# Kernel tuning notes

Measured on AMD Instinct MI355X. Metric: run time of the kernel, lower is better.

Reference implementation:

```python
import jax, jax.numpy as jnp
import numpy as np

B, S, D = 4, 4096, 256


def setup_inputs() -> dict:
    key = jax.random.key(0)
    ks = jax.random.split(key, 8)
    inv = 1.0 / np.sqrt(D)
    return {
        "input_tensor": jax.random.normal(ks[0], (B, S, D), dtype=jnp.float32),
        "attention_mask": jax.random.randint(ks[1], (B, S, S), 0, 2) == 1,
        "Wq": jax.random.uniform(ks[2], (D, D), jnp.float32, -inv, inv),
        "bq": jax.random.uniform(ks[3], (D,), jnp.float32, -inv, inv),
        "Wk": jax.random.uniform(ks[4], (D, D), jnp.float32, -inv, inv),
        "bk": jax.random.uniform(ks[5], (D,), jnp.float32, -inv, inv),
        "Wv": jax.random.uniform(ks[6], (D, D), jnp.float32, -inv, inv),
        "bv": jax.random.uniform(ks[7], (D,), jnp.float32, -inv, inv),
    }


def reference(input_tensor, attention_mask, Wq, bq, Wk, bk, Wv, bv):
    # Linear projections: y = x @ W.T + b  (nn.Linear convention, W is [out,in])
    query = jnp.einsum("bsd,ed->bse", input_tensor, Wq) + bq
    key = jnp.einsum("bsd,ed->bse", input_tensor, Wk) + bk
    value = jnp.einsum("bsd,ed->bse", input_tensor, Wv) + bv
    # Faithful quirk: original scales by sqrt(query.size(1)) == sqrt(seq_len)
    scale = jnp.asarray(query.shape[1], query.dtype) ** 0.5
    scores = jnp.einsum("bqd,bkd->bqk", query, key) / scale  # [B,S,S]
    scores = jnp.where(attention_mask, jnp.asarray(-1e9, scores.dtype), scores)
    attn = jax.nn.softmax(scores, axis=-1)
    # dropout with p=0.0 is identity (eval-mode reference)
    context = jnp.einsum("bqk,bkd->bqd", attn, value)
    return context
```

## Files before the change

kernel.cpp:

```cpp
#include <hip/hip_runtime.h>
#include <hip/hip_bf16.h>
#include <stdint.h>

#define BB 4
#define SS 4096
#define DD 256

typedef __attribute__((ext_vector_type(4))) float f32x4;
typedef __attribute__((ext_vector_type(8))) short s16x8;

__device__ __forceinline__ ushort f2bf(float f) {
  __hip_bfloat16 h = __float2bfloat16(f);
  return __builtin_bit_cast(ushort, h);
}

__global__ void convert_kernel(const float* __restrict__ X,
                               const float* __restrict__ Wq,
                               const float* __restrict__ Wk,
                               const float* __restrict__ Wv,
                               const float* __restrict__ bq,
                               const float* __restrict__ bk,
                               const float* __restrict__ bv,
                               ushort* __restrict__ Xb,
                               ushort* __restrict__ Wb,
                               float* __restrict__ bias) {
  int tid = blockIdx.x * blockDim.x + threadIdx.x;
  int stride = gridDim.x * blockDim.x;
  const int NX4 = (BB * SS * DD) / 4;
  for (int i = tid; i < NX4; i += stride) {
    float4 v = ((const float4*)X)[i];
    ushort4 o = { f2bf(v.x), f2bf(v.y), f2bf(v.z), f2bf(v.w) };
    ((ushort4*)Xb)[i] = o;
  }
  const int NW4 = (DD * DD) / 4;
  for (int i = tid; i < NW4; i += stride) {
    float4 a = ((const float4*)Wq)[i];
    float4 b = ((const float4*)Wk)[i];
    float4 c = ((const float4*)Wv)[i];
    ushort4 oa = { f2bf(a.x), f2bf(a.y), f2bf(a.z), f2bf(a.w) };
    ushort4 ob = { f2bf(b.x), f2bf(b.y), f2bf(b.z), f2bf(b.w) };
    ushort4 oc = { f2bf(c.x), f2bf(c.y), f2bf(c.z), f2bf(c.w) };
    ((ushort4*)Wb)[i]           = oa;
    ((ushort4*)Wb)[NW4 + i]     = ob;
    ((ushort4*)Wb)[2 * NW4 + i] = oc;
  }
  if (tid < DD) {
    bias[tid]          = bq[tid];
    bias[DD + tid]     = bk[tid];
    bias[2 * DD + tid] = bv[tid];
  }
}

#define LROW 40

__global__ __launch_bounds__(256) void proj_gemm(const ushort* __restrict__ Xb,
                                                 const ushort* __restrict__ Wb,
                                                 const float* __restrict__ bias,
                                                 ushort* __restrict__ Qb,
                                                 ushort* __restrict__ Kb,
                                                 ushort* __restrict__ Vt) {
  __shared__ ushort Al[128 * LROW];
  __shared__ ushort Bl[128 * LROW];
  const int m0 = blockIdx.x * 128;
  const int n0 = blockIdx.y * 128;
  const int t = threadIdx.x;
  const int lane = t & 63;
  const int w = t >> 6;
  const int wr = w & 1, wc = w >> 1;
  const int col = lane & 15;
  const int quad = lane >> 4;

  f32x4 acc[4][4];
#pragma unroll
  for (int i = 0; i < 4; i++)
#pragma unroll
    for (int j = 0; j < 4; j++) acc[i][j] = f32x4{0.f, 0.f, 0.f, 0.f};

  const int ci0 = t, ci1 = 256 + t;
  const int r0 = ci0 >> 2, c0 = ci0 & 3;
  const int r1 = ci1 >> 2, c1 = ci1 & 3;

  s16x8 pa0 = *(const s16x8*)(Xb + (m0 + r0) * DD + c0 * 8);
  s16x8 pa1 = *(const s16x8*)(Xb + (m0 + r1) * DD + c1 * 8);
  s16x8 pb0 = *(const s16x8*)(Wb + (n0 + r0) * DD + c0 * 8);
  s16x8 pb1 = *(const s16x8*)(Wb + (n0 + r1) * DD + c1 * 8);

  for (int kk = 0; kk < DD; kk += 32) {
    __syncthreads();
    *(s16x8*)&Al[r0 * LROW + c0 * 8] = pa0;
    *(s16x8*)&Al[r1 * LROW + c1 * 8] = pa1;
    *(s16x8*)&Bl[r0 * LROW + c0 * 8] = pb0;
    *(s16x8*)&Bl[r1 * LROW + c1 * 8] = pb1;
    __syncthreads();
    const int kn = kk + 32;
    if (kn < DD) {
      pa0 = *(const s16x8*)(Xb + (m0 + r0) * DD + kn + c0 * 8);
      pa1 = *(const s16x8*)(Xb + (m0 + r1) * DD + kn + c1 * 8);
      pb0 = *(const s16x8*)(Wb + (n0 + r0) * DD + kn + c0 * 8);
      pb1 = *(const s16x8*)(Wb + (n0 + r1) * DD + kn + c1 * 8);
    }
    s16x8 af[4], bfr[4];
#pragma unroll
    for (int mi = 0; mi < 4; mi++)
      af[mi] = *(const s16x8*)&Al[(wr * 64 + mi * 16 + col) * LROW + quad * 8];
#pragma unroll
    for (int ni = 0; ni < 4; ni++)
      bfr[ni] = *(const s16x8*)&Bl[(wc * 64 + ni * 16 + col) * LROW + quad * 8];
#pragma unroll
    for (int mi = 0; mi < 4; mi++)
#pragma unroll
      for (int ni = 0; ni < 4; ni++)
        acc[mi][ni] = __builtin_amdgcn_mfma_f32_16x16x32_bf16(af[mi], bfr[ni], acc[mi][ni], 0, 0, 0);
  }

  const int region = n0 >> 8;
#pragma unroll
  for (int mi = 0; mi < 4; mi++) {
    const int gm = m0 + wr * 64 + mi * 16 + quad * 4;
#pragma unroll
    for (int ni = 0; ni < 4; ni++) {
      const int gn = n0 + wc * 64 + ni * 16 + col;
      const float bb = bias[gn];
      f32x4 v = acc[mi][ni];
      if (region == 0) {
#pragma unroll
        for (int rg = 0; rg < 4; rg++)
          Qb[(gm + rg) * DD + gn] = f2bf((v[rg] + bb) * 0.015625f);
      } else if (region == 1) {
        const int d = gn - 256;
#pragma unroll
        for (int rg = 0; rg < 4; rg++)
          Kb[(gm + rg) * DD + d] = f2bf(v[rg] + bb);
      } else {
        const int d = gn - 512;
        const int b = gm >> 12;
        const int s = gm & (SS - 1);
        ushort4 o = { f2bf(v[0] + bb), f2bf(v[1] + bb), f2bf(v[2] + bb), f2bf(v[3] + bb) };
        *(ushort4*)&Vt[((size_t)(b << 8) + d) * SS + s] = o;
      }
    }
  }
}

#define NKT 32
#define KROW 264
#define VROW 40
#define PROW 40

__global__ __launch_bounds__(256) void attn_kernel(const ushort* __restrict__ Qb,
                                                   const ushort* __restrict__ Kb,
                                                   const ushort* __restrict__ Vt,
                                                   const int* __restrict__ mask,
                                                   float* __restrict__ out) {
  __shared__ ushort Kl[NKT * KROW];
  __shared__ ushort Vl[DD * VROW];
  __shared__ ushort Pl[4][16 * PROW];

  const int qt = blockIdx.x;
  const int b = blockIdx.y;
  const int t = threadIdx.x;
  const int lane = t & 63;
  const int w = t >> 6;
  const int col = lane & 15;
  const int quad = lane >> 4;

  const int q0 = qt * 64;
  const int qrow = q0 + w * 16;

  s16x8 qf[8];
  {
    const ushort* qp = Qb + ((size_t)b * SS + qrow + col) * DD + quad * 8;
#pragma unroll
    for (int dc = 0; dc < 8; dc++) qf[dc] = *(const s16x8*)(qp + dc * 32);
  }

  int kr[4], kc[4], vd[4], vc[4];
#pragma unroll
  for (int i = 0; i < 4; i++) {
    const int ci = i * 256 + t;
    kr[i] = ci >> 5; kc[i] = ci & 31;
    vd[i] = ci >> 2; vc[i] = ci & 3;
  }

  const ushort* Kg = Kb + (size_t)b * SS * DD;
  const ushort* Vg = Vt + (size_t)b * DD * SS;
  const int* Mg = mask + ((size_t)b * SS + q0 + w * 16 + quad * 4) * SS;

  f32x4 Oc[16];
#pragma unroll
  for (int i = 0; i < 16; i++) Oc[i] = f32x4{0.f, 0.f, 0.f, 0.f};
  float m_i[4] = {-INFINITY, -INFINITY, -INFINITY, -INFINITY};
  float l_i[4] = {0.f, 0.f, 0.f, 0.f};

  s16x8 pk[4], pv[4];
  int pm[2][4];
#pragma unroll
  for (int i = 0; i < 4; i++) {
    pk[i] = *(const s16x8*)(Kg + (size_t)kr[i] * DD + kc[i] * 8);
    pv[i] = *(const s16x8*)(Vg + (size_t)vd[i] * SS + vc[i] * 8);
  }
#pragma unroll
  for (int jt = 0; jt < 2; jt++)
#pragma unroll
    for (int rg = 0; rg < 4; rg++) pm[jt][rg] = Mg[rg * SS + jt * 16 + col];

  const int NT = SS / NKT;
  for (int tt = 0; tt < NT; tt++) {
    __syncthreads();
#pragma unroll
    for (int i = 0; i < 4; i++) {
      *(s16x8*)&Kl[kr[i] * KROW + kc[i] * 8] = pk[i];
      *(s16x8*)&Vl[vd[i] * VROW + vc[i] * 8] = pv[i];
    }
    __syncthreads();
    int mcur[2][4];
#pragma unroll
    for (int jt = 0; jt < 2; jt++)
#pragma unroll
      for (int rg = 0; rg < 4; rg++) mcur[jt][rg] = pm[jt][rg];
    if (tt + 1 < NT) {
      const int k0n = (tt + 1) * NKT;
#pragma unroll
      for (int i = 0; i < 4; i++) {
        pk[i] = *(const s16x8*)(Kg + ((size_t)k0n + kr[i]) * DD + kc[i] * 8);
        pv[i] = *(const s16x8*)(Vg + (size_t)vd[i] * SS + k0n + vc[i] * 8);
      }
#pragma unroll
      for (int jt = 0; jt < 2; jt++)
#pragma unroll
        for (int rg = 0; rg < 4; rg++) pm[jt][rg] = Mg[rg * SS + k0n + jt * 16 + col];
    }

    f32x4 st[2];
#pragma unroll
    for (int jt = 0; jt < 2; jt++) {
      f32x4 s = f32x4{0.f, 0.f, 0.f, 0.f};
#pragma unroll
      for (int dc = 0; dc < 8; dc++) {
        s16x8 kb = *(const s16x8*)&Kl[(jt * 16 + col) * KROW + dc * 32 + quad * 8];
        s = __builtin_amdgcn_mfma_f32_16x16x32_bf16(qf[dc], kb, s, 0, 0, 0);
      }
      st[jt] = s;
    }
#pragma unroll
    for (int jt = 0; jt < 2; jt++)
#pragma unroll
      for (int rg = 0; rg < 4; rg++)
        if (mcur[jt][rg]) st[jt][rg] = -1e9f;

    float al[4];
#pragma unroll
    for (int rg = 0; rg < 4; rg++) {
      float v = fmaxf(st[0][rg], st[1][rg]);
      v = fmaxf(v, __shfl_xor(v, 1));
      v = fmaxf(v, __shfl_xor(v, 2));
      v = fmaxf(v, __shfl_xor(v, 4));
      v = fmaxf(v, __shfl_xor(v, 8));
      const float mn = fmaxf(m_i[rg], v);
      al[rg] = __expf(m_i[rg] - mn);
      m_i[rg] = mn;
    }
#pragma unroll
    for (int rg = 0; rg < 4; rg++) {
      const float p0 = __expf(st[0][rg] - m_i[rg]);
      const float p1 = __expf(st[1][rg] - m_i[rg]);
      st[0][rg] = p0; st[1][rg] = p1;
      float s2 = p0 + p1;
      s2 += __shfl_xor(s2, 1);
      s2 += __shfl_xor(s2, 2);
      s2 += __shfl_xor(s2, 4);
      s2 += __shfl_xor(s2, 8);
      l_i[rg] = l_i[rg] * al[rg] + s2;
    }
#pragma unroll
    for (int dt = 0; dt < 16; dt++)
#pragma unroll
      for (int rg = 0; rg < 4; rg++) Oc[dt][rg] *= al[rg];

#pragma unroll
    for (int jt = 0; jt < 2; jt++)
#pragma unroll
      for (int rg = 0; rg < 4; rg++)
        Pl[w][(quad * 4 + rg) * PROW + jt * 16 + col] = f2bf(st[jt][rg]);
    s16x8 pa = *(const s16x8*)&Pl[w][col * PROW + quad * 8];

#pragma unroll
    for (int dt = 0; dt < 16; dt++) {
      s16x8 vb = *(const s16x8*)&Vl[(dt * 16 + col) * VROW + quad * 8];
      Oc[dt] = __builtin_amdgcn_mfma_f32_16x16x32_bf16(pa, vb, Oc[dt], 0, 0, 0);
    }
  }

  float inv[4];
#pragma unroll
  for (int rg = 0; rg < 4; rg++) inv[rg] = 1.0f / l_i[rg];
  float* op = out + ((size_t)b * SS + qrow + quad * 4) * DD;
#pragma unroll
  for (int dt = 0; dt < 16; dt++)
#pragma unroll
    for (int rg = 0; rg < 4; rg++)
      op[rg * DD + dt * 16 + col] = Oc[dt][rg] * inv[rg];
}

extern "C" void kernel_launch(void* const* d_in, const int* in_sizes, int n_in,
                              void* d_out, int out_size, void* d_ws, size_t ws_size,
                              hipStream_t stream) {
  const float* X  = (const float*)d_in[0];
  const int* mask = (const int*)d_in[1];
  const float* Wq = (const float*)d_in[2];
  const float* bq = (const float*)d_in[3];
  const float* Wk = (const float*)d_in[4];
  const float* bk = (const float*)d_in[5];
  const float* Wv = (const float*)d_in[6];
  const float* bv = (const float*)d_in[7];
  float* out = (float*)d_out;

  ushort* base = (ushort*)d_ws;
  ushort* Xb = base;
  ushort* Wb = Xb + (size_t)BB * SS * DD;
  ushort* Qb = Wb + (size_t)3 * DD * DD;
  ushort* Kb = Qb + (size_t)BB * SS * DD;
  ushort* Vt = Kb + (size_t)BB * SS * DD;
  float* bias = (float*)(Vt + (size_t)BB * SS * DD);

  convert_kernel<<<1024, 256, 0, stream>>>(X, Wq, Wk, Wv, bq, bk, bv, Xb, Wb, bias);
  proj_gemm<<<dim3(128, 6), 256, 0, stream>>>(Xb, Wb, bias, Qb, Kb, Vt);
  attn_kernel<<<dim3(64, 4), 256, 0, stream>>>(Qb, Kb, Vt, mask, out);
}
```

Measured before the change: 619.1 us.

## Split key range across two wave groups per block and merge softmax partials

Doubles the attention block to 512 threads, with each 256-thread group processing half of the key sequence using its own K/V LDS buffers. At the end, group 1 writes its running max, sum and output accumulators to LDS, and group 0 rescales and merges them before writing the output. This is meant to raise waves per CU, since the grid has only one block per CU, to better hide memory and MFMA latency. It also sets wave priority around the MFMA loops. The larger block tightens the per-thread register budget and adds a merge step.

```diff
diff --git a/kernel.cpp b/kernel.cpp
--- a/kernel.cpp
+++ b/kernel.cpp
@@ -147,22 +147,36 @@
 #define VROW 40
 #define PROW 40
 
-__global__ __launch_bounds__(256) void attn_kernel(const ushort* __restrict__ Qb,
+#define KL_U (NKT * KROW)
+#define VL_U (DD * VROW)
+#define PL_U (16 * PROW)
+#define VOFF (2 * KL_U)
+#define POFF (VOFF + 2 * VL_U)
+#define SM_U (POFF + 8 * PL_U)
+
+#define XSTRIDE 72
+
+__global__ __launch_bounds__(512) void attn_kernel(const ushort* __restrict__ Qb,
                                                    const ushort* __restrict__ Kb,
                                                    const ushort* __restrict__ Vt,
                                                    const int* __restrict__ mask,
                                                    float* __restrict__ out) {
-  __shared__ ushort Kl[NKT * KROW];
-  __shared__ ushort Vl[DD * VROW];
-  __shared__ ushort Pl[4][16 * PROW];
+  __shared__ __align__(16) ushort sm[SM_U];
 
   const int qt = blockIdx.x;
   const int b = blockIdx.y;
   const int t = threadIdx.x;
+  const int g = t >> 8;
+  const int tg = t & 255;
   const int lane = t & 63;
-  const int w = t >> 6;
+  const int w = tg >> 6;
+  const int w8 = t >> 6;
   const int col = lane & 15;
   const int quad = lane >> 4;
+
+  ushort* Kl = sm + g * KL_U;
+  ushort* Vl = sm + VOFF + g * VL_U;
+  ushort* Pw = sm + POFF + w8 * PL_U;
 
   const int q0 = qt * 64;
   const int qrow = q0 + w * 16;
@@ -177,14 +191,14 @@
   int kr[4], kc[4], vd[4], vc[4];
 #pragma unroll
   for (int i = 0; i < 4; i++) {
-    const int ci = i * 256 + t;
+    const int ci = i * 256 + tg;
     kr[i] = ci >> 5; kc[i] = ci & 31;
     vd[i] = ci >> 2; vc[i] = ci & 3;
   }
 
   const ushort* Kg = Kb + (size_t)b * SS * DD;
   const ushort* Vg = Vt + (size_t)b * DD * SS;
-  const int* Mg = mask + ((size_t)b * SS + q0 + w * 16 + quad * 4) * SS;
+  const int* Mg = mask + ((size_t)b * SS + qrow + quad * 4) * SS;
 
   f32x4 Oc[16];
 #pragma unroll
@@ -192,20 +206,22 @@
   float m_i[4] = {-INFINITY, -INFINITY, -INFINITY, -INFINITY};
   float l_i[4] = {0.f, 0.f, 0.f, 0.f};
 
+  const int NT2 = (SS / NKT) / 2;
+  const int kb0 = g * NT2 * NKT;
+
   s16x8 pk[4], pv[4];
   int pm[2][4];
 #pragma unroll
   for (int i = 0; i < 4; i++) {
-    pk[i] = *(const s16x8*)(Kg + (size_t)kr[i] * DD + kc[i] * 8);
-    pv[i] = *(const s16x8*)(Vg + (size_t)vd[i] * SS + vc[i] * 8);
+    pk[i] = *(const s16x8*)(Kg + (size_t)(kb0 + kr[i]) * DD + kc[i] * 8);
+    pv[i] = *(const s16x8*)(Vg + (size_t)vd[i] * SS + kb0 + vc[i] * 8);
   }
 #pragma unroll
   for (int jt = 0; jt < 2; jt++)
 #pragma unroll
-    for (int rg = 0; rg < 4; rg++) pm[jt][rg] = Mg[rg * SS + jt * 16 + col];
-
-  const int NT = SS / NKT;
-  for (int tt = 0; tt < NT; tt++) {
+    for (int rg = 0; rg < 4; rg++) pm[jt][rg] = Mg[rg * SS + kb0 + jt * 16 + col];
+
+  for (int tt = 0; tt < NT2; tt++) {
     __syncthreads();
 #pragma unroll
     for (int i = 0; i < 4; i++) {
@@ -218,8 +234,8 @@
     for (int jt = 0; jt < 2; jt++)
 #pragma unroll
       for (int rg = 0; rg < 4; rg++) mcur[jt][rg] = pm[jt][rg];
-    if (tt + 1 < NT) {
-      const int k0n = (tt + 1) * NKT;
+    if (tt + 1 < NT2) {
+      const int k0n = kb0 + (tt + 1) * NKT;
 #pragma unroll
       for (int i = 0; i < 4; i++) {
         pk[i] = *(const s16x8*)(Kg + ((size_t)k0n + kr[i]) * DD + kc[i] * 8);
@@ -232,6 +248,7 @@
     }
 
     f32x4 st[2];
+    __builtin_amdgcn_s_setprio(1);
 #pragma unroll
     for (int jt = 0; jt < 2; jt++) {
       f32x4 s = f32x4{0.f, 0.f, 0.f, 0.f};
@@ -242,6 +259,7 @@
       }
       st[jt] = s;
     }
+    __builtin_amdgcn_s_setprio(0);
 #pragma unroll
     for (int jt = 0; jt < 2; jt++)
 #pragma unroll
@@ -281,25 +299,48 @@
     for (int jt = 0; jt < 2; jt++)
 #pragma unroll
       for (int rg = 0; rg < 4; rg++)
-        Pl[w][(quad * 4 + rg) * PROW + jt * 16 + col] = f2bf(st[jt][rg]);
-    s16x8 pa = *(const s16x8*)&Pl[w][col * PROW + quad * 8];
-
+        Pw[(quad * 4 + rg) * PROW + jt * 16 + col] = f2bf(st[jt][rg]);
+    s16x8 pa = *(const s16x8*)&Pw[col * PROW + quad * 8];
+
+    __builtin_amdgcn_s_setprio(1);
 #pragma unroll
     for (int dt = 0; dt < 16; dt++) {
       s16x8 vb = *(const s16x8*)&Vl[(dt * 16 + col) * VROW + quad * 8];
       Oc[dt] = __builtin_amdgcn_mfma_f32_16x16x32_bf16(pa, vb, Oc[dt], 0, 0, 0);
     }
-  }
-
-  float inv[4];
-#pragma unroll
-  for (int rg = 0; rg < 4; rg++) inv[rg] = 1.0f / l_i[rg];
-  float* op = out + ((size_t)b * SS + qrow + quad * 4) * DD;
-#pragma unroll
-  for (int dt = 0; dt < 16; dt++)
-#pragma unroll
-    for (int rg = 0; rg < 4; rg++)
-      op[rg * DD + dt * 16 + col] = Oc[dt][rg] * inv[rg];
+    __builtin_amdgcn_s_setprio(0);
+  }
+
+  __syncthreads();
+  float* ex = (float*)sm;
+  float* slot = ex + (size_t)(w * 64 + lane) * XSTRIDE;
+  if (g == 1) {
+#pragma unroll
+    for (int rg = 0; rg < 4; rg++) { slot[rg] = m_i[rg]; slot[4 + rg] = l_i[rg]; }
+#pragma unroll
+    for (int dt = 0; dt < 16; dt++) *(f32x4*)&slot[8 + dt * 4] = Oc[dt];
+  }
+  __syncthreads();
+  if (g == 0) {
+    float a0[4], a1[4], inv[4];
+#pragma unroll
+    for (int rg = 0; rg < 4; rg++) {
+      const float m1 = slot[rg];
+      const float l1 = slot[4 + rg];
+      const float mm = fmaxf(m_i[rg], m1);
+      a0[rg] = __expf(m_i[rg] - mm);
+      a1[rg] = __expf(m1 - mm);
+      inv[rg] = 1.0f / (l_i[rg] * a0[rg] + l1 * a1[rg]);
+    }
+    float* op = out + ((size_t)b * SS + qrow + quad * 4) * DD;
+#pragma unroll
+    for (int dt = 0; dt < 16; dt++) {
+      const f32x4 o1 = *(const f32x4*)&slot[8 + dt * 4];
+#pragma unroll
+      for (int rg = 0; rg < 4; rg++)
+        op[rg * DD + dt * 16 + col] = (Oc[dt][rg] * a0[rg] + o1[rg] * a1[rg]) * inv[rg];
+    }
+  }
 }
 
 extern "C" void kernel_launch(void* const* d_in, const int* in_sizes, int n_in,
@@ -325,5 +366,5 @@
 
   convert_kernel<<<1024, 256, 0, stream>>>(X, Wq, Wk, Wv, bq, bk, bv, Xb, Wb, bias);
   proj_gemm<<<dim3(128, 6), 256, 0, stream>>>(Xb, Wb, bias, Qb, Kb, Vt);
-  attn_kernel<<<dim3(64, 4), 256, 0, stream>>>(Qb, Kb, Vt, mask, out);
-}
+  attn_kernel<<<dim3(64, 4), 512, 0, stream>>>(Qb, Kb, Vt, mask, out);
+}
```

Measured after the change: 524.3 us. 1.18x faster.
